# Kernel optimization log

Hardware: AMD Instinct MI355X
Metric: run time of the kernel (lower is better)

Reference implementation:

```python
import jax, jax.numpy as jnp
import numpy as np

NEG = -1e9

def setup_inputs() -> dict:
    key = jax.random.key(0)
    ks = jax.random.split(key, 6)
    B, T, H = 32, 2048, 1024
    dec = jax.random.normal(ks[0], (B, H), dtype=jnp.float32)
    enc = jax.random.normal(ks[1], (B, T, H), dtype=jnp.float32)
    mask = jax.random.randint(ks[2], (B, T), 0, 2).astype(jnp.int32)
    scale = 1.0 / np.sqrt(H)
    W_enc = jax.random.normal(ks[3], (H, H), dtype=jnp.float32) * scale
    W_dec = jax.random.normal(ks[4], (H, H), dtype=jnp.float32) * scale
    v = jax.random.normal(ks[5], (H,), dtype=jnp.float32) * scale
    return {"decoder_hidden": dec, "encoder_outputs": enc, "mask": mask,
            "W_enc": W_enc, "W_dec": W_dec, "v": v}

def reference(decoder_hidden, encoder_outputs, mask, W_enc, W_dec, v):
    # enc proj: [B,T,H] @ W_enc^T ; dec proj: [B,H] @ W_dec^T broadcast over T
    enc_p = jnp.einsum('bth,oh->bto', encoder_outputs, W_enc)
    dec_p = jnp.einsum('bh,oh->bo', decoder_hidden, W_dec)[:, None, :]  # [B,1,H]
    energy = jnp.tanh(enc_p + dec_p)                                    # [B,T,H]
    scores = jnp.einsum('bth,h->bt', energy, v)                         # [B,T]
    scores = jnp.where(mask == 0, NEG, scores)
    attn_weights = jax.nn.softmax(scores, axis=1)                       # [B,T]
    context = jnp.einsum('bt,bth->bh', attn_weights, encoder_outputs)   # [B,H]
    return (context, attn_weights)
```

## Files before the change

### kernel.cpp

```cpp
#include <hip/hip_runtime.h>
#include <hip/hip_bf16.h>
#include <stdint.h>

#define B_ 32
#define T_ 2048
#define H_ 1024
#define M_ (B_*T_)

typedef __bf16 bf16x8 __attribute__((ext_vector_type(8)));
typedef float  f32x4  __attribute__((ext_vector_type(4)));
typedef float  f32x16 __attribute__((ext_vector_type(16)));

__device__ __forceinline__ float tanh_fast(float x) {
    float e = __expf(2.0f * x);
    return 1.0f - 2.0f / (e + 1.0f);
}

__device__ __forceinline__ bf16x8 cvt2(f32x4 f0, f32x4 f1) {
    bf16x8 h;
    h[0] = (__bf16)f0[0]; h[1] = (__bf16)f0[1]; h[2] = (__bf16)f0[2]; h[3] = (__bf16)f0[3];
    h[4] = (__bf16)f1[0]; h[5] = (__bf16)f1[1]; h[6] = (__bf16)f1[2]; h[7] = (__bf16)f1[3];
    return h;
}

__device__ __forceinline__ void gl_lds16(const __bf16* g, __bf16* l) {
    __builtin_amdgcn_global_load_lds(
        (const __attribute__((address_space(1))) void*)g,
        (__attribute__((address_space(3))) void*)l, 16, 0, 0);
}

__global__ __launch_bounds__(256) void k_prep(const float* __restrict__ We,
                                              __bf16* __restrict__ Wt,
                                              const float* __restrict__ dec,
                                              const float* __restrict__ Wd,
                                              float* __restrict__ decp) {
    int bx = blockIdx.x;
    int tid = threadIdx.x;
    if (bx < 512) {
        int tg = bx * 256 + tid;
        int lane = tg & 63;
        int c = (tg >> 6) & 31;
        int s = tg >> 11;
        int o = c * 32 + (lane & 31);
        int k = s * 16 + (lane >> 5) * 8;
        const f32x4* src = (const f32x4*)&We[(size_t)o * H_ + k];
        *(bf16x8*)&Wt[(size_t)tg * 8] = cvt2(src[0], src[1]);
    } else {
        int bxd = bx - 512;
        int b = bxd & 31, oc = bxd >> 5;
        int o = oc * 64 + (tid >> 2);
        int kq = tid & 3;
        const f32x4* wr = (const f32x4*)&Wd[(size_t)o * H_ + kq * 256];
        const f32x4* dr = (const f32x4*)&dec[(size_t)b * H_ + kq * 256];
        f32x4 s4 = {0.f, 0.f, 0.f, 0.f};
#pragma unroll 8
        for (int i = 0; i < 64; ++i) s4 += wr[i] * dr[i];
        float s = s4[0] + s4[1] + s4[2] + s4[3];
        s += __shfl_xor(s, 1);
        s += __shfl_xor(s, 2);
        if (kq == 0) decp[b * H_ + o] = s;
    }
}

__global__ __launch_bounds__(256) void k_prep_enc(const float* __restrict__ enc,
                                                  __bf16* __restrict__ enc_t) {
    int bx = blockIdx.x;
    int rg = bx >> 1, rt = bx & 1;
    int tid = threadIdx.x;
    int w = tid >> 6, lane = tid & 63;
    int l5 = lane & 31, sh = lane >> 5;
    int row = rg * 64 + rt * 32 + l5;
    const float* src = &enc[(size_t)row * H_];
#pragma unroll 2
    for (int i = 0; i < 8; ++i) {
        int s = (w + 4 * i) * 2 + sh;
        const f32x4* s4 = (const f32x4*)(src + s * 16);
        bf16x8 h0 = cvt2(s4[0], s4[1]);
        bf16x8 h1 = cvt2(s4[2], s4[3]);
        size_t base = ((size_t)(rg * 64 + s) * 2 + rt) * 64;
        *(bf16x8*)&enc_t[(base + l5) * 8]      = h0;
        *(bf16x8*)&enc_t[(base + 32 + l5) * 8] = h1;
    }
}

__global__ __launch_bounds__(256, 4) void k_scores(const __bf16* __restrict__ enc_t,
                                                   const float* __restrict__ decp,
                                                   const __bf16* __restrict__ Wt,
                                                   const float* __restrict__ v,
                                                   float* __restrict__ scores_p) {
    __shared__ __bf16 A_lds[2][8192];
    __shared__ float red[4][64];

    const int tid = threadIdx.x;
    const int w = tid >> 6, lane = tid & 63;
    const int l5 = lane & 31, q2 = lane >> 5;

    const int bx = blockIdx.x;
    const int xs = bx & 7;
    const int q = bx >> 3;
    const int nt = q & 3;
    const int rg = (q >> 2) * 8 + xs;
    const int m0 = rg * 64;
    const int b = m0 >> 11;
    const int cg0 = nt * 8 + w * 2;

    float dp[2], vvv[2];
#pragma unroll
    for (int ct = 0; ct < 2; ++ct) {
        int col = (cg0 + ct) * 32 + l5;
        dp[ct]  = decp[b * H_ + col];
        vvv[ct] = v[col];
    }

    f32x16 acc[2][2];
#pragma unroll
    for (int rt = 0; rt < 2; ++rt)
#pragma unroll
        for (int ct = 0; ct < 2; ++ct)
#pragma unroll
            for (int g = 0; g < 16; ++g)
                acc[rt][ct][g] = dp[ct];

    const __bf16* gsrc = enc_t + (size_t)rg * 65536 + (size_t)tid * 8;

#pragma unroll
    for (int i = 0; i < 4; ++i)
        gl_lds16(gsrc + i * 2048, &A_lds[0][(i * 256 + tid) * 8]);

    bf16x8 bb[2][2];
#pragma unroll
    for (int p = 0; p < 2; ++p)
#pragma unroll
        for (int ct = 0; ct < 2; ++ct)
            bb[p][ct] = *(const bf16x8*)&Wt[(((size_t)p * 32 + cg0 + ct) * 64 + lane) * 8];

    __syncthreads();

    int buf = 0;
#pragma unroll 1
    for (int ck = 0; ck < 8; ++ck) {
        if (ck < 7) {
            const __bf16* gs = gsrc + (size_t)(ck + 1) * 8192;
            __bf16* dst = A_lds[buf ^ 1];
#pragma unroll
            for (int i = 0; i < 4; ++i)
                gl_lds16(gs + i * 2048, &dst[(i * 256 + tid) * 8]);
        }

        const __bf16* bufp = A_lds[buf];

        bf16x8 af[2][2];
#pragma unroll
        for (int p = 0; p < 2; ++p)
#pragma unroll
            for (int rt = 0; rt < 2; ++rt)
                af[p][rt] = *(const bf16x8*)&bufp[((p * 2 + rt) * 64 + lane) * 8];

#pragma unroll
        for (int sl = 0; sl < 8; ++sl) {
            const int s = ck * 8 + sl;
            bf16x8 a0 = af[sl & 1][0], a1 = af[sl & 1][1];
            bf16x8 w0 = bb[sl & 1][0], w1 = bb[sl & 1][1];

            {
                int sn = (s + 2) & 63;
#pragma unroll
                for (int ct = 0; ct < 2; ++ct)
                    bb[sl & 1][ct] = *(const bf16x8*)&Wt[(((size_t)sn * 32 + cg0 + ct) * 64 + lane) * 8];
            }
            if (sl < 6) {
                int sl2 = sl + 2;
#pragma unroll
                for (int rt = 0; rt < 2; ++rt)
                    af[sl & 1][rt] = *(const bf16x8*)&bufp[((sl2 * 2 + rt) * 64 + lane) * 8];
            }

            acc[0][0] = __builtin_amdgcn_mfma_f32_32x32x16_bf16(a0, w0, acc[0][0], 0, 0, 0);
            acc[0][1] = __builtin_amdgcn_mfma_f32_32x32x16_bf16(a0, w1, acc[0][1], 0, 0, 0);
            acc[1][0] = __builtin_amdgcn_mfma_f32_32x32x16_bf16(a1, w0, acc[1][0], 0, 0, 0);
            acc[1][1] = __builtin_amdgcn_mfma_f32_32x32x16_bf16(a1, w1, acc[1][1], 0, 0, 0);
        }

        __syncthreads();
        buf ^= 1;
    }

    float sp[2][16];
#pragma unroll
    for (int rt = 0; rt < 2; ++rt)
#pragma unroll
        for (int g = 0; g < 16; ++g)
            sp[rt][g] = tanh_fast(acc[rt][0][g]) * vvv[0] + tanh_fast(acc[rt][1][g]) * vvv[1];

#pragma unroll
    for (int rt = 0; rt < 2; ++rt)
#pragma unroll
        for (int g = 0; g < 16; ++g) {
            float s = sp[rt][g];
            s += __shfl_xor(s, 1);
            s += __shfl_xor(s, 2);
            s += __shfl_xor(s, 4);
            s += __shfl_xor(s, 8);
            s += __shfl_xor(s, 16);
            sp[rt][g] = s;
        }

    if (l5 == 0) {
#pragma unroll
        for (int rt = 0; rt < 2; ++rt)
#pragma unroll
            for (int g = 0; g < 16; ++g) {
                int row = rt * 32 + (g & 3) + 8 * (g >> 2) + 4 * q2;
                red[w][row] = sp[rt][g];
            }
    }
    __syncthreads();
    if (tid < 64) {
        float s = red[0][tid] + red[1][tid] + red[2][tid] + red[3][tid];
        scores_p[nt * M_ + m0 + tid] = s;
    }
}

__global__ __launch_bounds__(256) void k_softmax(const float* __restrict__ scores_p,
                                                 const int* __restrict__ mask,
                                                 float* __restrict__ attn) {
    int b = blockIdx.x;
    int tid = threadIdx.x;
    int w = tid >> 6, lane = tid & 63;
    __shared__ float sm[2][4];
    float val[8];
    float mx = -3e38f;
#pragma unroll
    for (int ii = 0; ii < 8; ++ii) {
        int idx = b * T_ + tid + ii * 256;
        float s = scores_p[idx] + scores_p[M_ + idx] + scores_p[2 * M_ + idx] + scores_p[3 * M_ + idx];
        s = (mask[idx] == 0) ? -1e9f : s;
        val[ii] = s;
        mx = fmaxf(mx, s);
    }
#pragma unroll
    for (int m = 1; m <= 32; m <<= 1) mx = fmaxf(mx, __shfl_xor(mx, m));
    if (lane == 0) sm[0][w] = mx;
    __syncthreads();
    mx = fmaxf(fmaxf(sm[0][0], sm[0][1]), fmaxf(sm[0][2], sm[0][3]));
    float lsum = 0.f;
#pragma unroll
    for (int ii = 0; ii < 8; ++ii) {
        val[ii] = __expf(val[ii] - mx);
        lsum += val[ii];
    }
#pragma unroll
    for (int m = 1; m <= 32; m <<= 1) lsum += __shfl_xor(lsum, m);
    if (lane == 0) sm[1][w] = lsum;
    __syncthreads();
    float inv = 1.0f / (sm[1][0] + sm[1][1] + sm[1][2] + sm[1][3]);
#pragma unroll
    for (int ii = 0; ii < 8; ++ii)
        attn[b * T_ + tid + ii * 256] = val[ii] * inv;
}

__global__ __launch_bounds__(256) void k_context(const float* __restrict__ enc,
                                                 const float* __restrict__ attn,
                                                 float* __restrict__ ctxp) {
    int bx = blockIdx.x;
    int b = bx >> 5, seg = bx & 31;
    int t0 = seg * 64;
    const float* ep = &enc[((size_t)b * T_ + t0) * H_ + threadIdx.x * 4];
    const float* ap = &attn[b * T_ + t0];
    f32x4 acc = {0.f, 0.f, 0.f, 0.f};
#pragma unroll 8
    for (int t = 0; t < 64; ++t) {
        float a = ap[t];
        acc += a * *(const f32x4*)(ep + (size_t)t * H_);
    }
    *(f32x4*)&ctxp[((size_t)seg * B_ + b) * H_ + threadIdx.x * 4] = acc;
}

__global__ __launch_bounds__(256) void k_ctxred(const float* __restrict__ ctxp,
                                                float* __restrict__ ctx) {
    int i = blockIdx.x * 256 + threadIdx.x;
    float s = 0.f;
#pragma unroll
    for (int sg = 0; sg < 32; ++sg)
        s += ctxp[(size_t)sg * (B_ * H_) + i];
    ctx[i] = s;
}

extern "C" void kernel_launch(void* const* d_in, const int* in_sizes, int n_in,
                              void* d_out, int out_size, void* d_ws, size_t ws_size,
                              hipStream_t stream) {
    (void)in_sizes; (void)n_in; (void)out_size; (void)ws_size;
    const float* dec  = (const float*)d_in[0];
    const float* enc  = (const float*)d_in[1];
    const int*   mask = (const int*)d_in[2];
    const float* We   = (const float*)d_in[3];
    const float* Wd   = (const float*)d_in[4];
    const float* v    = (const float*)d_in[5];

    float* out = (float*)d_out;
    char* ws = (char*)d_ws;
    float*  decp     = (float*)ws;
    float*  scores_p = (float*)(ws + 131072);
    __bf16* Wt       = (__bf16*)(ws + 131072 + 1048576);
    __bf16* enc_t    = (__bf16*)(ws + 131072 + 1048576 + 2097152);
    float*  ctxp     = (float*)(ws + 131072 + 1048576 + 2097152);

    k_prep    <<<1024, 256, 0, stream>>>(We, Wt, dec, Wd, decp);
    k_prep_enc<<<2048, 256, 0, stream>>>(enc, enc_t);
    k_scores  <<<4096, 256, 0, stream>>>(enc_t, decp, Wt, v, scores_p);
    k_softmax <<<32, 256, 0, stream>>>(scores_p, mask, out + B_ * H_);
    k_context <<<1024, 256, 0, stream>>>(enc, out + B_ * H_, ctxp);
    k_ctxred  <<<128, 256, 0, stream>>>(ctxp, out);
}
```

Baseline: 626.7 us.

## Fuse enc bf16 conversion into scores GEMM and softmax into context kernel

Removes the separate encoder fp32-to-bf16 pre-transpose kernel. The scores GEMM now streams fp32 encoder rows straight into swizzled LDS through a triple-buffered pipeline and converts to bf16 when reading fragments. The softmax is also fused into the context kernel, with each block recomputing the softmax for its batch and using its own weight segment from LDS, and the number of context segments drops to 16. This avoids a full write and reread of the bf16 encoder copy and two launches, at the cost of twice the LDS traffic per tile, conversion work inside the GEMM loop, lower occupancy, and the softmax being computed redundantly in every block.

```diff
diff --git a/kernel.cpp b/kernel.cpp
--- a/kernel.cpp
+++ b/kernel.cpp
@@ -23,7 +23,7 @@
     return h;
 }
 
-__device__ __forceinline__ void gl_lds16(const __bf16* g, __bf16* l) {
+__device__ __forceinline__ void gl_lds16f(const float* g, float* l) {
     __builtin_amdgcn_global_load_lds(
         (const __attribute__((address_space(1))) void*)g,
         (__attribute__((address_space(3))) void*)l, 16, 0, 0);
@@ -62,33 +62,12 @@
     }
 }
 
-__global__ __launch_bounds__(256) void k_prep_enc(const float* __restrict__ enc,
-                                                  __bf16* __restrict__ enc_t) {
-    int bx = blockIdx.x;
-    int rg = bx >> 1, rt = bx & 1;
-    int tid = threadIdx.x;
-    int w = tid >> 6, lane = tid & 63;
-    int l5 = lane & 31, sh = lane >> 5;
-    int row = rg * 64 + rt * 32 + l5;
-    const float* src = &enc[(size_t)row * H_];
-#pragma unroll 2
-    for (int i = 0; i < 8; ++i) {
-        int s = (w + 4 * i) * 2 + sh;
-        const f32x4* s4 = (const f32x4*)(src + s * 16);
-        bf16x8 h0 = cvt2(s4[0], s4[1]);
-        bf16x8 h1 = cvt2(s4[2], s4[3]);
-        size_t base = ((size_t)(rg * 64 + s) * 2 + rt) * 64;
-        *(bf16x8*)&enc_t[(base + l5) * 8]      = h0;
-        *(bf16x8*)&enc_t[(base + 32 + l5) * 8] = h1;
-    }
-}
-
-__global__ __launch_bounds__(256, 4) void k_scores(const __bf16* __restrict__ enc_t,
+__global__ __launch_bounds__(256, 3) void k_scores(const float* __restrict__ enc,
                                                    const float* __restrict__ decp,
                                                    const __bf16* __restrict__ Wt,
                                                    const float* __restrict__ v,
                                                    float* __restrict__ scores_p) {
-    __shared__ __bf16 A_lds[2][8192];
+    __shared__ float A_lds[3 * 4096];
     __shared__ float red[4][64];
 
     const int tid = threadIdx.x;
@@ -121,69 +100,75 @@
             for (int g = 0; g < 16; ++g)
                 acc[rt][ct][g] = dp[ct];
 
-    const __bf16* gsrc = enc_t + (size_t)rg * 65536 + (size_t)tid * 8;
-
-#pragma unroll
-    for (int i = 0; i < 4; ++i)
-        gl_lds16(gsrc + i * 2048, &A_lds[0][(i * 256 + tid) * 8]);
-
-    bf16x8 bb[2][2];
-#pragma unroll
-    for (int p = 0; p < 2; ++p)
-#pragma unroll
-        for (int ct = 0; ct < 2; ++ct)
-            bb[p][ct] = *(const bf16x8*)&Wt[(((size_t)p * 32 + cg0 + ct) * 64 + lane) * 8];
-
-    __syncthreads();
-
-    int buf = 0;
+    const int srow = w * 16 + (lane >> 4);
+    const int sof  = ((lane & 15) * 4) ^ ((srow & 7) << 2);
+    const int ld0  = w * 4 * 256 + lane * 4;
+
+#define STAGE(ck_, cb_) do { \
+    _Pragma("unroll") \
+    for (int i_ = 0; i_ < 4; ++i_) { \
+        int row_ = srow + 4 * i_; \
+        int of_  = sof ^ ((i_ & 1) << 4); \
+        gl_lds16f(enc + (size_t)(m0 + row_) * H_ + (ck_) * 64 + of_, \
+                  &A_lds[(cb_) * 4096 + ld0 + i_ * 256]); \
+    } } while (0)
+
+    bf16x8 bb[4][2];
+#define BLOAD(ck_) do { \
+    _Pragma("unroll") \
+    for (int sl_ = 0; sl_ < 4; ++sl_) \
+        _Pragma("unroll") \
+        for (int ct_ = 0; ct_ < 2; ++ct_) \
+            bb[sl_][ct_] = *(const bf16x8*)&Wt[(((size_t)((ck_) * 4 + sl_) * 32 + cg0 + ct_) * 64 + lane) * 8]; \
+    } while (0)
+
+    STAGE(0, 0);
+    STAGE(1, 1);
+    STAGE(2, 2);
+    BLOAD(0);
+    __builtin_amdgcn_sched_barrier(0);
+    asm volatile("s_waitcnt vmcnt(8)" ::: "memory");
+    __builtin_amdgcn_s_barrier();
+    __builtin_amdgcn_sched_barrier(0);
+
+    int cb = 0;
 #pragma unroll 1
-    for (int ck = 0; ck < 8; ++ck) {
-        if (ck < 7) {
-            const __bf16* gs = gsrc + (size_t)(ck + 1) * 8192;
-            __bf16* dst = A_lds[buf ^ 1];
-#pragma unroll
-            for (int i = 0; i < 4; ++i)
-                gl_lds16(gs + i * 2048, &dst[(i * 256 + tid) * 8]);
+    for (int ck = 0; ck < 16; ++ck) {
+        const float* bufp = &A_lds[cb * 4096];
+
+#pragma unroll
+        for (int sl = 0; sl < 4; ++sl) {
+            bf16x8 a[2];
+#pragma unroll
+            for (int rt = 0; rt < 2; ++rt) {
+                int row = rt * 32 + l5;
+                int kf  = sl * 16 + q2 * 8;
+                int sw  = (row & 7) << 2;
+                f32x4 lo = *(const f32x4*)&bufp[row * 64 + (kf ^ sw)];
+                f32x4 hi = *(const f32x4*)&bufp[row * 64 + ((kf + 4) ^ sw)];
+                a[rt] = cvt2(lo, hi);
+            }
+            acc[0][0] = __builtin_amdgcn_mfma_f32_32x32x16_bf16(a[0], bb[sl][0], acc[0][0], 0, 0, 0);
+            acc[0][1] = __builtin_amdgcn_mfma_f32_32x32x16_bf16(a[0], bb[sl][1], acc[0][1], 0, 0, 0);
+            acc[1][0] = __builtin_amdgcn_mfma_f32_32x32x16_bf16(a[1], bb[sl][0], acc[1][0], 0, 0, 0);
+            acc[1][1] = __builtin_amdgcn_mfma_f32_32x32x16_bf16(a[1], bb[sl][1], acc[1][1], 0, 0, 0);
         }
 
-        const __bf16* bufp = A_lds[buf];
-
-        bf16x8 af[2][2];
-#pragma unroll
-        for (int p = 0; p < 2; ++p)
-#pragma unroll
-            for (int rt = 0; rt < 2; ++rt)
-                af[p][rt] = *(const bf16x8*)&bufp[((p * 2 + rt) * 64 + lane) * 8];
-
-#pragma unroll
-        for (int sl = 0; sl < 8; ++sl) {
-            const int s = ck * 8 + sl;
-            bf16x8 a0 = af[sl & 1][0], a1 = af[sl & 1][1];
-            bf16x8 w0 = bb[sl & 1][0], w1 = bb[sl & 1][1];
-
-            {
-                int sn = (s + 2) & 63;
-#pragma unroll
-                for (int ct = 0; ct < 2; ++ct)
-                    bb[sl & 1][ct] = *(const bf16x8*)&Wt[(((size_t)sn * 32 + cg0 + ct) * 64 + lane) * 8];
-            }
-            if (sl < 6) {
-                int sl2 = sl + 2;
-#pragma unroll
-                for (int rt = 0; rt < 2; ++rt)
-                    af[sl & 1][rt] = *(const bf16x8*)&bufp[((sl2 * 2 + rt) * 64 + lane) * 8];
-            }
-
-            acc[0][0] = __builtin_amdgcn_mfma_f32_32x32x16_bf16(a0, w0, acc[0][0], 0, 0, 0);
-            acc[0][1] = __builtin_amdgcn_mfma_f32_32x32x16_bf16(a0, w1, acc[0][1], 0, 0, 0);
-            acc[1][0] = __builtin_amdgcn_mfma_f32_32x32x16_bf16(a1, w0, acc[1][0], 0, 0, 0);
-            acc[1][1] = __builtin_amdgcn_mfma_f32_32x32x16_bf16(a1, w1, acc[1][1], 0, 0, 0);
-        }
-
-        __syncthreads();
-        buf ^= 1;
-    }
+        __builtin_amdgcn_sched_barrier(0);
+        asm volatile("" ::: "memory");
+        __builtin_amdgcn_s_barrier();
+        asm volatile("" ::: "memory");
+        __builtin_amdgcn_sched_barrier(0);
+
+        if (ck < 15) BLOAD(ck + 1);
+        __builtin_amdgcn_sched_barrier(0);
+        if (ck < 13) STAGE(ck + 3, cb);
+        __builtin_amdgcn_sched_barrier(0);
+
+        cb = cb + 1; if (cb == 3) cb = 0;
+    }
+#undef STAGE
+#undef BLOAD
 
     float sp[2][16];
 #pragma unroll
@@ -205,6 +190,7 @@
             sp[rt][g] = s;
         }
 
+    __syncthreads();
     if (l5 == 0) {
 #pragma unroll
         for (int rt = 0; rt < 2; ++rt)
@@ -221,13 +207,18 @@
     }
 }
 
-__global__ __launch_bounds__(256) void k_softmax(const float* __restrict__ scores_p,
-                                                 const int* __restrict__ mask,
-                                                 float* __restrict__ attn) {
-    int b = blockIdx.x;
+__global__ __launch_bounds__(256) void k_ctx(const float* __restrict__ scores_p,
+                                             const int* __restrict__ mask,
+                                             const float* __restrict__ enc,
+                                             float* __restrict__ attn,
+                                             float* __restrict__ ctxp) {
+    int bx = blockIdx.x;
+    int b = bx >> 4, seg = bx & 15;
     int tid = threadIdx.x;
     int w = tid >> 6, lane = tid & 63;
     __shared__ float sm[2][4];
+    __shared__ float wa[128];
+
     float val[8];
     float mx = -3e38f;
 #pragma unroll
@@ -254,34 +245,35 @@
     if (lane == 0) sm[1][w] = lsum;
     __syncthreads();
     float inv = 1.0f / (sm[1][0] + sm[1][1] + sm[1][2] + sm[1][3]);
-#pragma unroll
-    for (int ii = 0; ii < 8; ++ii)
-        attn[b * T_ + tid + ii * 256] = val[ii] * inv;
-}
-
-__global__ __launch_bounds__(256) void k_context(const float* __restrict__ enc,
-                                                 const float* __restrict__ attn,
-                                                 float* __restrict__ ctxp) {
-    int bx = blockIdx.x;
-    int b = bx >> 5, seg = bx & 31;
-    int t0 = seg * 64;
-    const float* ep = &enc[((size_t)b * T_ + t0) * H_ + threadIdx.x * 4];
-    const float* ap = &attn[b * T_ + t0];
+
+    if (seg == 0) {
+#pragma unroll
+        for (int ii = 0; ii < 8; ++ii)
+            attn[b * T_ + tid + ii * 256] = val[ii] * inv;
+    }
+    {
+        int half = seg & 1, ii0 = seg >> 1;
+        if ((tid >> 7) == half) wa[tid & 127] = val[ii0] * inv;
+    }
+    __syncthreads();
+
+    int t0 = seg * 128;
+    const float* ep = &enc[((size_t)b * T_ + t0) * H_ + tid * 4];
     f32x4 acc = {0.f, 0.f, 0.f, 0.f};
 #pragma unroll 8
-    for (int t = 0; t < 64; ++t) {
-        float a = ap[t];
+    for (int t = 0; t < 128; ++t) {
+        float a = wa[t];
         acc += a * *(const f32x4*)(ep + (size_t)t * H_);
     }
-    *(f32x4*)&ctxp[((size_t)seg * B_ + b) * H_ + threadIdx.x * 4] = acc;
-}
-
-__global__ __launch_bounds__(256) void k_ctxred(const float* __restrict__ ctxp,
-                                                float* __restrict__ ctx) {
+    *(f32x4*)&ctxp[((size_t)(seg * B_ + b)) * H_ + tid * 4] = acc;
+}
+
+__global__ __launch_bounds__(256) void k_red(const float* __restrict__ ctxp,
+                                             float* __restrict__ ctx) {
     int i = blockIdx.x * 256 + threadIdx.x;
     float s = 0.f;
 #pragma unroll
-    for (int sg = 0; sg < 32; ++sg)
+    for (int sg = 0; sg < 16; ++sg)
         s += ctxp[(size_t)sg * (B_ * H_) + i];
     ctx[i] = s;
 }
@@ -302,13 +294,10 @@
     float*  decp     = (float*)ws;
     float*  scores_p = (float*)(ws + 131072);
     __bf16* Wt       = (__bf16*)(ws + 131072 + 1048576);
-    __bf16* enc_t    = (__bf16*)(ws + 131072 + 1048576 + 2097152);
     float*  ctxp     = (float*)(ws + 131072 + 1048576 + 2097152);
 
-    k_prep    <<<1024, 256, 0, stream>>>(We, Wt, dec, Wd, decp);
-    k_prep_enc<<<2048, 256, 0, stream>>>(enc, enc_t);
-    k_scores  <<<4096, 256, 0, stream>>>(enc_t, decp, Wt, v, scores_p);
-    k_softmax <<<32, 256, 0, stream>>>(scores_p, mask, out + B_ * H_);
-    k_context <<<1024, 256, 0, stream>>>(enc, out + B_ * H_, ctxp);
-    k_ctxred  <<<128, 256, 0, stream>>>(ctxp, out);
-}
+    k_prep  <<<1024, 256, 0, stream>>>(We, Wt, dec, Wd, decp);
+    k_scores<<<4096, 256, 0, stream>>>(enc, decp, Wt, v, scores_p);
+    k_ctx   <<<512, 256, 0, stream>>>(scores_p, mask, enc, out + B_ * H_, ctxp);
+    k_red   <<<128, 256, 0, stream>>>(ctxp, out);
+}
```

Result: faster. 569.8 us (-9.1%).
